# Kernel tuning notes

Hardware: AMD Instinct MI355X
Metric: run time of the kernel (lower is better)

The kernel has to match this reference:

```python
import jax, jax.numpy as jnp
import numpy as np

BETA_F = 1000.0
BETA_B = 1.0
CLAMP = 12.0
B, C, H, W = 4, 1, 1024, 1024
N_NODES = 262144  # nodes per max-tree


def soft_mask(logits):
    # forward sigmoid with beta_f gain and +-12 clamp (clamp_logits=True)
    return jax.nn.sigmoid(jnp.clip(BETA_F * logits, -CLAMP, CLAMP))


def tree_filter(sigma, levels, parent):
    """Differentiable connected filtering on one max-tree.
    Node value = level(root) + sum over root->node path of sigma_j*(level_j - level_parent_j),
    computed with pointer-doubling ancestor sums (log N gather passes).
    sigma, levels: (N,), parent: (N,) int32 with parent[0]==0 (root).
    """
    N = sigma.shape[0]
    delta = levels - levels[parent]          # per-node gray-level increment
    c = (sigma * delta).at[0].set(levels[0])  # root contributes its level
    # sentinel node N with contribution 0 and self-pointer, terminates chains
    acc = jnp.concatenate([c, jnp.zeros((1,), c.dtype)])
    ptr = jnp.concatenate([parent.at[0].set(N), jnp.full((1,), N, parent.dtype)])
    steps = int(np.ceil(np.log2(N))) + 1
    for _ in range(steps):
        acc, ptr = acc + acc[ptr], ptr[ptr]
    return acc[:N]


def setup_inputs() -> dict:
    rng = np.random.default_rng(0)
    T = B * C  # one tree per (b, c) image
    idx = np.arange(N_NODES)
    # topologically ordered random tree: parent[i] in [0, i), parent[0] = 0
    parent = np.floor(rng.random((T, N_NODES)) * idx).astype(np.int32)
    # monotone increasing gray levels: ancestor-sum of positive increments
    inc = (rng.random((T, N_NODES)) + 0.1).astype(np.float32)
    acc = np.concatenate([inc, np.zeros((T, 1), np.float32)], 1)
    ptr = np.concatenate([parent, np.full((T, 1), N_NODES, np.int64)], 1)
    ptr[:, 0] = N_NODES
    for _ in range(int(np.ceil(np.log2(N_NODES))) + 1):
        acc = acc + np.take_along_axis(acc, ptr, 1)
        ptr = np.take_along_axis(ptr, ptr, 1)
    levels = acc[:, :N_NODES]
    attr_norm = rng.random((T, N_NODES)).astype(np.float32)  # minmax01-normalized attribute
    pixel_to_node = rng.integers(0, N_NODES, (T, H * W)).astype(np.int32)
    x = rng.standard_normal((B, C, H, W)).astype(np.float32)
    return {
        "x": jnp.asarray(x),
        "attr_norm": jnp.asarray(attr_norm),
        "levels": jnp.asarray(levels),
        "thr": jnp.full((1,), 0.5, jnp.float32),  # torch init.constant_(p, 0.5)
        "parent": jnp.asarray(parent),
        "pixel_to_node": jnp.asarray(pixel_to_node),
    }


def reference(x, attr_norm, levels, thr, parent, pixel_to_node):
    # logits = attr_scaled - threshold_norm, per node, per tree
    sigma = soft_mask(attr_norm - thr.reshape(()))          # (T, N)
    v = jax.vmap(tree_filter)(sigma, levels, parent)         # (T, N) filtered node values
    y = jnp.take_along_axis(v, pixel_to_node, axis=1)        # node -> pixel gather
    return y.reshape(B, C, H, W)  # top_hat=False, num_groups=1 -> out_channels=C
```

## Files before the change

### kernel.cpp

```cpp
#include <hip/hip_runtime.h>

#define NT 4
#define NN 262144
#define NMASK (NN - 1)
#define HW 1048576
#define KPRE 16384

#define SWIZ(b, tree, chunk)                \
    int tree  = ((b) & 7) >> 1;             \
    int chunk = (((b) >> 3) << 1) | ((b) & 1);

__global__ __launch_bounds__(256) void k_build(const float* __restrict__ attr,
                                               const float* __restrict__ levels,
                                               const float* __restrict__ thr,
                                               const int* __restrict__ parent,
                                               int2* __restrict__ cmb) {
    SWIZ(blockIdx.x, tree, chunk)
    int n = chunk * 256 + threadIdx.x;
    int i = (tree << 18) + n;
    int p = parent[i] & NMASK;
    float lv = levels[i];
    float lp = levels[(tree << 18) | p];
    float z = 1000.0f * (attr[i] - thr[0]);
    z = fminf(fmaxf(z, -12.0f), 12.0f);
    float s = 1.0f / (1.0f + __expf(-z));
    float c = s * (lv - lp);
    if (n == 0) { c = lv; p = 0; }
    cmb[i] = make_int2(p, __float_as_int(c));
}

__global__ __launch_bounds__(256) void k_prefix(const int2* __restrict__ cmb,
                                                float* __restrict__ v) {
    SWIZ(blockIdx.x, tree, chunk)
    int node = chunk * 256 + threadIdx.x;
    const int2* ctree = cmb + (tree << 18);
    float acc = 0.0f;
    int cur = node;
    bool alive = true;
    for (int it = 0; it < 64 && __any(alive); ++it) {
        if (alive) {
            int2 rec = ctree[cur];
            acc += __int_as_float(rec.y);
            if (cur == 0) alive = false;
            else cur = rec.x;
        }
    }
    v[(tree << 18) + node] = acc;
}

__global__ __launch_bounds__(256) void k_walk(const int2* __restrict__ cmb,
                                              float* __restrict__ v) {
    SWIZ(blockIdx.x, tree, chunk)
    int base = KPRE + chunk * 1024;
    const int2*  ctree = cmb + (tree << 18);
    const float* vtree = v + (tree << 18);

    int   cur[4];
    float acc[4];
    int alive = 0xF;
#pragma unroll
    for (int k = 0; k < 4; ++k) {
        cur[k] = base + threadIdx.x + k * 256;
        acc[k] = 0.0f;
    }
    for (int it = 0; it < 64 && __any(alive); ++it) {
#pragma unroll
        for (int k = 0; k < 4; ++k) {
            if (alive & (1 << k)) {
                int2 rec = ctree[cur[k]];
                acc[k] += __int_as_float(rec.y);
                int nxt = rec.x;
                if (nxt < KPRE) {
                    acc[k] += vtree[nxt];
                    alive &= ~(1 << k);
                } else {
                    cur[k] = nxt;
                }
            }
        }
    }
#pragma unroll
    for (int k = 0; k < 4; ++k)
        v[(tree << 18) + base + threadIdx.x + k * 256] = acc[k];
}

__global__ __launch_bounds__(256) void k_pix(const float* __restrict__ v,
                                             const int* __restrict__ p2n,
                                             float* __restrict__ y) {
    SWIZ(blockIdx.x, tree, chunk)
    int i = (tree << 18) + chunk * 256 + threadIdx.x;
    int4 idx = ((const int4*)p2n)[i];
    const float* vt = v + (tree << 18);
    float4 o;
    o.x = vt[idx.x & NMASK];
    o.y = vt[idx.y & NMASK];
    o.z = vt[idx.z & NMASK];
    o.w = vt[idx.w & NMASK];
    ((float4*)y)[i] = o;
}

extern "C" void kernel_launch(void* const* d_in, const int* in_sizes, int n_in,
                              void* d_out, int out_size, void* d_ws, size_t ws_size,
                              hipStream_t stream) {
    const float* attr   = (const float*)d_in[1];
    const float* levels = (const float*)d_in[2];
    const float* thr    = (const float*)d_in[3];
    const int*   parent = (const int*)d_in[4];
    const int*   p2n    = (const int*)d_in[5];
    float*       y      = (float*)d_out;

    int2*  cmb = (int2*)d_ws;
    float* v   = (float*)((char*)d_ws + (size_t)NT * NN * sizeof(int2));

    k_build <<<NT * NN / 256, 256, 0, stream>>>(attr, levels, thr, parent, cmb);
    k_prefix<<<NT * KPRE / 256, 256, 0, stream>>>(cmb, v);
    k_walk  <<<NT * (NN - KPRE) / 1024, 256, 0, stream>>>(cmb, v);
    k_pix   <<<NT * HW / 4 / 256, 256, 0, stream>>>(v, p2n, y);
}
```

Measured before the change: 135.5 us.

## Claim work dynamically by XCD, stage prefix tree in LDS, vectorize build

Blocks now claim tree chunks dynamically through atomic counters, preferring the tree that matches their XCD id, so each tree's data stays in one XCD's L2. The prefix stage shrinks to 8192 nodes per tree and runs one 1024-thread block per tree with parents and contributions held in shared memory. The build kernel processes four nodes per thread with vector loads and stores. This adds a memset and per-block atomics, and it leaves only four blocks to do the serial prefix work.

```diff
diff --git a/kernel.cpp b/kernel.cpp
--- a/kernel.cpp
+++ b/kernel.cpp
@@ -4,74 +4,130 @@
 #define NN 262144
 #define NMASK (NN - 1)
 #define HW 1048576
-#define KPRE 16384
+#define KPRE 8192
+#define CNT_OFF (12 << 20)
 
-#define SWIZ(b, tree, chunk)                \
-    int tree  = ((b) & 7) >> 1;             \
-    int chunk = (((b) >> 3) << 1) | ((b) & 1);
+__device__ __forceinline__ int xcd_pref() {
+    int x;
+    asm volatile("s_getreg_b32 %0, hwreg(HW_REG_XCC_ID)" : "=s"(x));
+    return (x & 7) >> 1;
+}
+
+__device__ __forceinline__ int claim_chunk(int* cnt, int limit, int pref, int* tree_out) {
+    for (int d = 0; d < 4; ++d) {
+        int t = (pref + d) & 3;
+        int c = atomicAdd(&cnt[t * 16], 1);
+        if (c < limit) { *tree_out = t; return c; }
+    }
+    return -1;
+}
 
 __global__ __launch_bounds__(256) void k_build(const float* __restrict__ attr,
                                                const float* __restrict__ levels,
                                                const float* __restrict__ thr,
                                                const int* __restrict__ parent,
-                                               int2* __restrict__ cmb) {
-    SWIZ(blockIdx.x, tree, chunk)
-    int n = chunk * 256 + threadIdx.x;
-    int i = (tree << 18) + n;
-    int p = parent[i] & NMASK;
-    float lv = levels[i];
-    float lp = levels[(tree << 18) | p];
-    float z = 1000.0f * (attr[i] - thr[0]);
-    z = fminf(fmaxf(z, -12.0f), 12.0f);
-    float s = 1.0f / (1.0f + __expf(-z));
-    float c = s * (lv - lp);
-    if (n == 0) { c = lv; p = 0; }
-    cmb[i] = make_int2(p, __float_as_int(c));
+                                               int2* __restrict__ cmb,
+                                               int* __restrict__ cnt) {
+    __shared__ int s_tree, s_chunk;
+    if (threadIdx.x == 0) {
+        int tr, ck = claim_chunk(cnt, 256, xcd_pref(), &tr);
+        s_tree = tr; s_chunk = ck;
+    }
+    __syncthreads();
+    if (s_chunk < 0) return;
+    int tree = s_tree, tbase = tree << 18;
+    int idx4 = s_chunk * 256 + threadIdx.x;
+    int n0 = idx4 * 4;
+
+    int4   p4 = ((const int4*)(parent + tbase))[idx4];
+    float4 a4 = ((const float4*)(attr + tbase))[idx4];
+    float4 l4 = ((const float4*)(levels + tbase))[idx4];
+    float t0 = thr[0];
+
+    int   pe[4] = {p4.x & NMASK, p4.y & NMASK, p4.z & NMASK, p4.w & NMASK};
+    float ae[4] = {a4.x, a4.y, a4.z, a4.w};
+    float le[4] = {l4.x, l4.y, l4.z, l4.w};
+    int   oc[8];
+#pragma unroll
+    for (int e = 0; e < 4; ++e) {
+        float lp = levels[tbase + pe[e]];
+        float z = 1000.0f * (ae[e] - t0);
+        z = fminf(fmaxf(z, -12.0f), 12.0f);
+        float s = 1.0f / (1.0f + __expf(-z));
+        float c = s * (le[e] - lp);
+        int p = pe[e];
+        if (n0 + e == 0) { c = le[e]; p = 0; }
+        oc[2 * e] = p; oc[2 * e + 1] = __float_as_int(c);
+    }
+    int4* dst = (int4*)(cmb + tbase);
+    dst[2 * idx4]     = make_int4(oc[0], oc[1], oc[2], oc[3]);
+    dst[2 * idx4 + 1] = make_int4(oc[4], oc[5], oc[6], oc[7]);
 }
 
-__global__ __launch_bounds__(256) void k_prefix(const int2* __restrict__ cmb,
-                                                float* __restrict__ v) {
-    SWIZ(blockIdx.x, tree, chunk)
-    int node = chunk * 256 + threadIdx.x;
-    const int2* ctree = cmb + (tree << 18);
-    float acc = 0.0f;
-    int cur = node;
-    bool alive = true;
+__global__ __launch_bounds__(1024) void k_prefix(const int2* __restrict__ cmb,
+                                                 float* __restrict__ v) {
+    __shared__ int   ps[KPRE];
+    __shared__ float cs[KPRE];
+    int tree = blockIdx.x;
+    const int2* ct = cmb + (tree << 18);
+    for (int j = threadIdx.x; j < KPRE; j += 1024) {
+        int2 r = ct[j];
+        ps[j] = r.x;
+        cs[j] = __int_as_float(r.y);
+    }
+    __syncthreads();
+
+    int   cur[8];
+    float acc[8];
+    int alive = 0xFF;
+#pragma unroll
+    for (int k = 0; k < 8; ++k) { cur[k] = threadIdx.x + k * 1024; acc[k] = 0.0f; }
     for (int it = 0; it < 64 && __any(alive); ++it) {
-        if (alive) {
-            int2 rec = ctree[cur];
-            acc += __int_as_float(rec.y);
-            if (cur == 0) alive = false;
-            else cur = rec.x;
+#pragma unroll
+        for (int k = 0; k < 8; ++k) {
+            if (alive & (1 << k)) {
+                int c_ = cur[k];
+                acc[k] += cs[c_];
+                if (c_ == 0) alive &= ~(1 << k);
+                else cur[k] = ps[c_];
+            }
         }
     }
-    v[(tree << 18) + node] = acc;
+#pragma unroll
+    for (int k = 0; k < 8; ++k)
+        v[(tree << 18) + threadIdx.x + k * 1024] = acc[k];
 }
 
 __global__ __launch_bounds__(256) void k_walk(const int2* __restrict__ cmb,
-                                              float* __restrict__ v) {
-    SWIZ(blockIdx.x, tree, chunk)
-    int base = KPRE + chunk * 1024;
-    const int2*  ctree = cmb + (tree << 18);
-    const float* vtree = v + (tree << 18);
+                                              float* __restrict__ v,
+                                              int* __restrict__ cnt) {
+    __shared__ int s_tree, s_chunk;
+    if (threadIdx.x == 0) {
+        int tr, ck = claim_chunk(cnt + 64, (NN - KPRE) / 1024, xcd_pref(), &tr);
+        s_tree = tr; s_chunk = ck;
+    }
+    __syncthreads();
+    if (s_chunk < 0) return;
+    int tree = s_tree;
+    int base = KPRE + s_chunk * 1024;
+    const int2*  ct = cmb + (tree << 18);
+    const float* vt = v + (tree << 18);
 
     int   cur[4];
     float acc[4];
     int alive = 0xF;
 #pragma unroll
-    for (int k = 0; k < 4; ++k) {
-        cur[k] = base + threadIdx.x + k * 256;
-        acc[k] = 0.0f;
-    }
+    for (int k = 0; k < 4; ++k) { cur[k] = base + threadIdx.x + k * 256; acc[k] = 0.0f; }
+
     for (int it = 0; it < 64 && __any(alive); ++it) {
 #pragma unroll
         for (int k = 0; k < 4; ++k) {
             if (alive & (1 << k)) {
-                int2 rec = ctree[cur[k]];
+                int2 rec = ct[cur[k]];
                 acc[k] += __int_as_float(rec.y);
                 int nxt = rec.x;
                 if (nxt < KPRE) {
-                    acc[k] += vtree[nxt];
+                    acc[k] += vt[nxt];
                     alive &= ~(1 << k);
                 } else {
                     cur[k] = nxt;
@@ -86,17 +142,25 @@
 
 __global__ __launch_bounds__(256) void k_pix(const float* __restrict__ v,
                                              const int* __restrict__ p2n,
-                                             float* __restrict__ y) {
-    SWIZ(blockIdx.x, tree, chunk)
-    int i = (tree << 18) + chunk * 256 + threadIdx.x;
-    int4 idx = ((const int4*)p2n)[i];
+                                             float* __restrict__ y,
+                                             int* __restrict__ cnt) {
+    __shared__ int s_tree, s_chunk;
+    if (threadIdx.x == 0) {
+        int tr, ck = claim_chunk(cnt + 128, HW / 1024, xcd_pref(), &tr);
+        s_tree = tr; s_chunk = ck;
+    }
+    __syncthreads();
+    if (s_chunk < 0) return;
+    int tree = s_tree;
+    int i4 = (tree << 18) + s_chunk * 256 + threadIdx.x;
+    int4 idx = ((const int4*)p2n)[i4];
     const float* vt = v + (tree << 18);
     float4 o;
     o.x = vt[idx.x & NMASK];
     o.y = vt[idx.y & NMASK];
     o.z = vt[idx.z & NMASK];
     o.w = vt[idx.w & NMASK];
-    ((float4*)y)[i] = o;
+    ((float4*)y)[i4] = o;
 }
 
 extern "C" void kernel_launch(void* const* d_in, const int* in_sizes, int n_in,
@@ -110,10 +174,13 @@
     float*       y      = (float*)d_out;
 
     int2*  cmb = (int2*)d_ws;
-    float* v   = (float*)((char*)d_ws + (size_t)NT * NN * sizeof(int2));
+    float* v   = (float*)((char*)d_ws + (size_t)NT * NN * 8);
+    int*   cnt = (int*)((char*)d_ws + CNT_OFF);
 
-    k_build <<<NT * NN / 256, 256, 0, stream>>>(attr, levels, thr, parent, cmb);
-    k_prefix<<<NT * KPRE / 256, 256, 0, stream>>>(cmb, v);
-    k_walk  <<<NT * (NN - KPRE) / 1024, 256, 0, stream>>>(cmb, v);
-    k_pix   <<<NT * HW / 4 / 256, 256, 0, stream>>>(v, p2n, y);
+    hipMemsetAsync(cnt, 0, 192 * sizeof(int), stream);
+
+    k_build <<<NT * NN / 1024, 256, 0, stream>>>(attr, levels, thr, parent, cmb, cnt);
+    k_prefix<<<NT, 1024, 0, stream>>>(cmb, v);
+    k_walk  <<<NT * (NN - KPRE) / 1024, 256, 0, stream>>>(cmb, v, cnt);
+    k_pix   <<<NT * HW / 1024, 256, 0, stream>>>(v, p2n, y, cnt);
 }
```

New measurement: 175.7 us. +29.6%, slower.

## Fuse prefix walk into build kernel using LDS-resident top subtree

Applied to the files above, without the earlier changes.

Removes the separate prefix kernel. The first 32 blocks of the build kernel load the top KPRE nodes of their tree into LDS, compute node contributions there, and walk ancestor chains in shared memory to produce the prefix values directly. The remaining blocks build the combined parent/contribution records with 4-wide vectorized loads and stores. KPRE is halved so the prefix region fits in LDS, which pushes more chain-walking work into the global-memory walk kernel. Each prefix block also recomputes the full per-tree LDS table, so that work is duplicated eight times per tree.

```diff
diff --git a/kernel.cpp b/kernel.cpp
--- a/kernel.cpp
+++ b/kernel.cpp
@@ -4,7 +4,7 @@
 #define NN 262144
 #define NMASK (NN - 1)
 #define HW 1048576
-#define KPRE 16384
+#define KPRE 8192
 
 #define SWIZ(b, tree, chunk)                \
     int tree  = ((b) & 7) >> 1;             \
@@ -14,64 +14,112 @@
                                                const float* __restrict__ levels,
                                                const float* __restrict__ thr,
                                                const int* __restrict__ parent,
-                                               int2* __restrict__ cmb) {
-    SWIZ(blockIdx.x, tree, chunk)
-    int n = chunk * 256 + threadIdx.x;
-    int i = (tree << 18) + n;
-    int p = parent[i] & NMASK;
-    float lv = levels[i];
-    float lp = levels[(tree << 18) | p];
-    float z = 1000.0f * (attr[i] - thr[0]);
-    z = fminf(fmaxf(z, -12.0f), 12.0f);
-    float s = 1.0f / (1.0f + __expf(-z));
-    float c = s * (lv - lp);
-    if (n == 0) { c = lv; p = 0; }
-    cmb[i] = make_int2(p, __float_as_int(c));
-}
+                                               int2* __restrict__ cmb,
+                                               float* __restrict__ v) {
+    __shared__ float lvcs[KPRE];
+    __shared__ unsigned short ps[KPRE];
 
-__global__ __launch_bounds__(256) void k_prefix(const int2* __restrict__ cmb,
-                                                float* __restrict__ v) {
-    SWIZ(blockIdx.x, tree, chunk)
-    int node = chunk * 256 + threadIdx.x;
-    const int2* ctree = cmb + (tree << 18);
-    float acc = 0.0f;
-    int cur = node;
-    bool alive = true;
-    for (int it = 0; it < 64 && __any(alive); ++it) {
-        if (alive) {
-            int2 rec = ctree[cur];
-            acc += __int_as_float(rec.y);
-            if (cur == 0) alive = false;
-            else cur = rec.x;
+    int b = blockIdx.x;
+    if (b < 32) {
+        int tree = (b & 7) >> 1;
+        int sub  = ((b >> 3) << 1) | (b & 1);
+        int tbase = tree << 18;
+        float t0 = thr[0];
+
+        for (int j = threadIdx.x; j < KPRE; j += 256) {
+            lvcs[j] = levels[tbase + j];
+            ps[j] = (unsigned short)(parent[tbase + j] & (KPRE - 1));
         }
+        __syncthreads();
+
+        float creg[32];
+#pragma unroll
+        for (int k = 0; k < 32; ++k) {
+            int j = threadIdx.x + k * 256;
+            float lv = lvcs[j];
+            float lp = lvcs[ps[j]];
+            float z = 1000.0f * (attr[tbase + j] - t0);
+            z = fminf(fmaxf(z, -12.0f), 12.0f);
+            float s = 1.0f / (1.0f + __expf(-z));
+            creg[k] = (j == 0) ? lv : s * (lv - lp);
+        }
+        __syncthreads();
+#pragma unroll
+        for (int k = 0; k < 32; ++k) lvcs[threadIdx.x + k * 256] = creg[k];
+        __syncthreads();
+
+        int   cur[4];
+        float acc[4];
+        int alive = 0xF;
+#pragma unroll
+        for (int k = 0; k < 4; ++k) { cur[k] = sub * 1024 + threadIdx.x + k * 256; acc[k] = 0.0f; }
+        for (int it = 0; it < 64 && __any(alive); ++it) {
+#pragma unroll
+            for (int k = 0; k < 4; ++k) {
+                if (alive & (1 << k)) {
+                    int c_ = cur[k];
+                    acc[k] += lvcs[c_];
+                    if (c_ == 0) alive &= ~(1 << k);
+                    else cur[k] = ps[c_];
+                }
+            }
+        }
+#pragma unroll
+        for (int k = 0; k < 4; ++k)
+            v[tbase + sub * 1024 + threadIdx.x + k * 256] = acc[k];
+        return;
     }
-    v[(tree << 18) + node] = acc;
+
+    int g = b - 32;
+    SWIZ(g, tree, chunk0)
+    int chunk = 8 + chunk0;
+    int tbase = tree << 18;
+    int idx4 = chunk * 256 + threadIdx.x;
+    int4   p4 = ((const int4*)(parent + tbase))[idx4];
+    float4 a4 = ((const float4*)(attr + tbase))[idx4];
+    float4 l4 = ((const float4*)(levels + tbase))[idx4];
+    float t0 = thr[0];
+
+    int   pe[4] = {p4.x & NMASK, p4.y & NMASK, p4.z & NMASK, p4.w & NMASK};
+    float ae[4] = {a4.x, a4.y, a4.z, a4.w};
+    float le[4] = {l4.x, l4.y, l4.z, l4.w};
+    int   oc[8];
+#pragma unroll
+    for (int e = 0; e < 4; ++e) {
+        float lp = levels[tbase + pe[e]];
+        float z = 1000.0f * (ae[e] - t0);
+        z = fminf(fmaxf(z, -12.0f), 12.0f);
+        float s = 1.0f / (1.0f + __expf(-z));
+        oc[2 * e] = pe[e];
+        oc[2 * e + 1] = __float_as_int(s * (le[e] - lp));
+    }
+    int4* dst = (int4*)(cmb + tbase);
+    dst[2 * idx4]     = make_int4(oc[0], oc[1], oc[2], oc[3]);
+    dst[2 * idx4 + 1] = make_int4(oc[4], oc[5], oc[6], oc[7]);
 }
 
 __global__ __launch_bounds__(256) void k_walk(const int2* __restrict__ cmb,
                                               float* __restrict__ v) {
     SWIZ(blockIdx.x, tree, chunk)
     int base = KPRE + chunk * 1024;
-    const int2*  ctree = cmb + (tree << 18);
-    const float* vtree = v + (tree << 18);
+    const int2*  ct = cmb + (tree << 18);
+    const float* vt = v + (tree << 18);
 
     int   cur[4];
     float acc[4];
     int alive = 0xF;
 #pragma unroll
-    for (int k = 0; k < 4; ++k) {
-        cur[k] = base + threadIdx.x + k * 256;
-        acc[k] = 0.0f;
-    }
+    for (int k = 0; k < 4; ++k) { cur[k] = base + threadIdx.x + k * 256; acc[k] = 0.0f; }
+
     for (int it = 0; it < 64 && __any(alive); ++it) {
 #pragma unroll
         for (int k = 0; k < 4; ++k) {
             if (alive & (1 << k)) {
-                int2 rec = ctree[cur[k]];
+                int2 rec = ct[cur[k]];
                 acc[k] += __int_as_float(rec.y);
                 int nxt = rec.x;
                 if (nxt < KPRE) {
-                    acc[k] += vtree[nxt];
+                    acc[k] += vt[nxt];
                     alive &= ~(1 << k);
                 } else {
                     cur[k] = nxt;
@@ -88,15 +136,15 @@
                                              const int* __restrict__ p2n,
                                              float* __restrict__ y) {
     SWIZ(blockIdx.x, tree, chunk)
-    int i = (tree << 18) + chunk * 256 + threadIdx.x;
-    int4 idx = ((const int4*)p2n)[i];
+    int i4 = (tree << 18) + chunk * 256 + threadIdx.x;
+    int4 idx = ((const int4*)p2n)[i4];
     const float* vt = v + (tree << 18);
     float4 o;
     o.x = vt[idx.x & NMASK];
     o.y = vt[idx.y & NMASK];
     o.z = vt[idx.z & NMASK];
     o.w = vt[idx.w & NMASK];
-    ((float4*)y)[i] = o;
+    ((float4*)y)[i4] = o;
 }
 
 extern "C" void kernel_launch(void* const* d_in, const int* in_sizes, int n_in,
@@ -110,10 +158,9 @@
     float*       y      = (float*)d_out;
 
     int2*  cmb = (int2*)d_ws;
-    float* v   = (float*)((char*)d_ws + (size_t)NT * NN * sizeof(int2));
+    float* v   = (float*)((char*)d_ws + (size_t)NT * NN * 8);
 
-    k_build <<<NT * NN / 256, 256, 0, stream>>>(attr, levels, thr, parent, cmb);
-    k_prefix<<<NT * KPRE / 256, 256, 0, stream>>>(cmb, v);
-    k_walk  <<<NT * (NN - KPRE) / 1024, 256, 0, stream>>>(cmb, v);
-    k_pix   <<<NT * HW / 4 / 256, 256, 0, stream>>>(v, p2n, y);
+    k_build<<<32 + NT * (NN - KPRE) / 1024, 256, 0, stream>>>(attr, levels, thr, parent, cmb, v);
+    k_walk <<<NT * (NN - KPRE) / 1024, 256, 0, stream>>>(cmb, v);
+    k_pix  <<<NT * HW / 1024, 256, 0, stream>>>(v, p2n, y);
 }
```

Result: slower. 142.0 us (+4.8%).
